# Performance work log

Measured on AMD Instinct MI355X. Metric: run time of the kernel, lower is better.

Reference implementation:

```python
import jax, jax.numpy as jnp
import numpy as np

D, DEPTH, HEADS, P, IMG = 768, 12, 12, 16, 224
GRID = IMG // P
NTOK = GRID * GRID + 1  # 197
PLEN, NTASK, NCLS = 5, 5, 100
DEEP = (2, 3, 4)
HD = D // HEADS
LN_EPS = 1e-6


def _ln(x, w, b):
    m = x.mean(-1, keepdims=True)
    v = ((x - m) ** 2).mean(-1, keepdims=True)
    return (x - m) * jax.lax.rsqrt(v + LN_EPS) * w + b


def _l2n(x):
    return x * jax.lax.rsqrt(jnp.maximum((x * x).sum(-1, keepdims=True), 1e-12))


def _mlp(x, w1, b1, w2, b2):
    return jax.nn.gelu(x @ w1.T + b1, approximate=False) @ w2.T + b2


def _mha(x, wqkv, bqkv, wp, bp):
    B, N, _ = x.shape
    qkv = (x @ wqkv.T + bqkv).reshape(B, N, 3, HEADS, HD)
    q, k, v = qkv[:, :, 0], qkv[:, :, 1], qkv[:, :, 2]
    a = jax.nn.softmax(jnp.einsum('bnhd,bmhd->bhnm', q * HD ** -0.5, k), -1)
    o = jnp.einsum('bhnm,bmhd->bnhd', a, v).reshape(B, N, D)
    return o @ wp.T + bp


def _block(x, i, p):
    x = x + _mha(_ln(x, p['ln1_w'][i], p['ln1_b'][i]), p['qkv_w'][i], p['qkv_b'][i], p['proj_w'][i], p['proj_b'][i])
    return x + _mlp(_ln(x, p['ln2_w'][i], p['ln2_b'][i]), p['fc1_w'][i], p['fc1_b'][i], p['fc2_w'][i], p['fc2_b'][i])


def _blocks(x, p):
    for i in range(DEPTH):
        x = _block(x, i, p)
    return x


def _deep_block(x, i, li, prompts, p):
    # single-head prefix-prompt attention exactly as written in the torch module,
    # including the (buggy but faithful) transpose(1,2).reshape(B,N,C) scramble
    B, N, _ = x.shape
    nx = _ln(x, p['ln1_w'][i], p['ln1_b'][i])
    qkv = (nx @ p['qkv_w'][i].T + p['qkv_b'][i]).reshape(B, N, 3, D)
    q, k, v = qkv[:, :, 0], qkv[:, :, 1], qkv[:, :, 2]
    k = jnp.concatenate([prompts[:, 2 * li], k], axis=1)
    v = jnp.concatenate([prompts[:, 2 * li + 1], v], axis=1)
    a = jax.nn.softmax(jnp.einsum('bnd,bmd->bnm', q, k) * HD ** -0.5, -1)
    av = jnp.einsum('bnm,bmd->bnd', a, v)
    av = av.swapaxes(1, 2).reshape(B, N, D)
    x = x + (av @ p['proj_w'][i].T + p['proj_b'][i])
    return x + _mlp(_ln(x, p['ln2_w'][i], p['ln2_b'][i]), p['fc1_w'][i], p['fc1_b'][i], p['fc2_w'][i], p['fc2_b'][i])


def _embed(inputs, patch_w, patch_b, cls_token, pos_embed):
    B = inputs.shape[0]
    x = inputs.reshape(B, 3, GRID, P, GRID, P).transpose(0, 2, 4, 1, 3, 5).reshape(B, GRID * GRID, 3 * P * P)
    x = x @ patch_w.T + patch_b
    x = jnp.concatenate([jnp.broadcast_to(cls_token, (B, 1, D)), x], axis=1)
    return x + pos_embed


def _branch_forward(x, sel_main, main_idx, sub_idx, p, main_prompts, sub_prompt, pos_embed, fc_w, fc_b, norm_w, norm_b):
    B = x.shape[0]
    # ---- main branch: per-sample gathered deep prompts ----
    mx = x[main_idx]
    mp = main_prompts[sel_main].reshape(mx.shape[0], 2 * len(DEEP), PLEN, D)
    for i in range(DEPTH):
        if i in DEEP:
            mx = _deep_block(mx, i, DEEP.index(i), mp, p)
        else:
            mx = _block(mx, i, p)
    mx = _ln(mx, norm_w, norm_b)
    mlog = mx[:, 0] @ fc_w.T + fc_b  # fc_norm is Identity in timm vit_base
    # ---- sub branch: prepend sub prompts after cls ----
    sx = x[sub_idx]
    sp = jnp.broadcast_to(sub_prompt[0] + pos_embed[0, 0], (sx.shape[0], PLEN, D))
    sx = jnp.concatenate([sx[:, :1], sp, sx[:, 1:]], axis=1)
    sx = _ln(_blocks(sx, p), norm_w, norm_b)
    slog = sx[:, 1:1 + PLEN].mean(axis=1) @ fc_w.T + fc_b
    # scatter back to per-sample logits (fixed output shape)
    return jnp.zeros((B, NCLS), x.dtype).at[main_idx].set(mlog).at[sub_idx].set(slog)


def setup_inputs() -> dict:
    key = jax.random.key(0)
    ks = iter(jax.random.split(key, 32))
    nk = lambda: next(ks)
    r = lambda shape, sc=0.02: jax.random.normal(nk(), shape, jnp.float32) * sc
    return {
        'inputs': jax.random.normal(nk(), (16, 3, IMG, IMG), jnp.float32),
        'task_id': 4,
        'patch_w': r((D, 3 * P * P)),
        'patch_b': jnp.zeros((D,)),
        'cls_token': r((1, 1, D)),
        'pos_embed': r((1, NTOK, D)),
        'qkv_w': r((DEPTH, 3 * D, D)),
        'qkv_b': jnp.zeros((DEPTH, 3 * D)),
        'proj_w': r((DEPTH, D, D)),
        'proj_b': jnp.zeros((DEPTH, D)),
        'ln1_w': jnp.ones((DEPTH, D)), 'ln1_b': jnp.zeros((DEPTH, D)),
        'ln2_w': jnp.ones((DEPTH, D)), 'ln2_b': jnp.zeros((DEPTH, D)),
        'fc1_w': r((DEPTH, 4 * D, D)),
        'fc1_b': jnp.zeros((DEPTH, 4 * D)),
        'fc2_w': r((DEPTH, D, 4 * D)),
        'fc2_b': jnp.zeros((DEPTH, D)),
        'norm_w': jnp.ones((D,)), 'norm_b': jnp.zeros((D,)),
        'fc_w': r((NCLS, D)),
        'fc_b': jnp.zeros((NCLS,)),
        'main_key': r((NTASK, D), 1.0),
        'sub_key': r((1, D), 1.0),
        'main_prompts': r((NTASK, 1, 2, len(DEEP), PLEN, D), 1.0),
        'sub_prompt': r((1, PLEN, D), 1.0),
    }


def reference(inputs, task_id, patch_w, patch_b, cls_token, pos_embed, qkv_w, qkv_b, proj_w, proj_b,
              ln1_w, ln1_b, ln2_w, ln2_b, fc1_w, fc1_b, fc2_w, fc2_b, norm_w, norm_b, fc_w, fc_b,
              main_key, sub_key, main_prompts, sub_prompt):
    p = dict(qkv_w=qkv_w, qkv_b=qkv_b, proj_w=proj_w, proj_b=proj_b, ln1_w=ln1_w, ln1_b=ln1_b,
             ln2_w=ln2_w, ln2_b=ln2_b, fc1_w=fc1_w, fc1_b=fc1_b, fc2_w=fc2_w, fc2_b=fc2_b)
    x = _embed(inputs, patch_w, patch_b, cls_token, pos_embed)
    # frozen query pass (torch.no_grad in the original)
    query = _ln(_blocks(x, p), norm_w, norm_b)[:, 0]
    # test-time routing: cosine similarity to [main_key[:task_id+1], sub_key]
    cand = jnp.concatenate([main_key[:task_id + 1], sub_key], axis=0)
    sim = _l2n(query) @ _l2n(cand).T
    sel = jnp.argmax(sim, axis=1)  # selection_size == 1
    main_mask = sel <= task_id
    main_idx = jnp.nonzero(main_mask)[0]
    sub_idx = jnp.nonzero(jnp.logical_not(main_mask))[0]
    sel_main = sel[main_idx]
    return _branch_forward(x, sel_main, main_idx, sub_idx, p, main_prompts, sub_prompt, pos_embed,
                           fc_w, fc_b, norm_w, norm_b)
```

## Files before the change

### kernel.cpp

```cpp
#include <hip/hip_runtime.h>
#include <math.h>

#define B_    16
#define NT_   197
#define NS_   202
#define HEADS_ 12
#define DEPTH_ 12
#define NCLS_ 100
#define MROW_ (B_ * NT_)
#define SROW_ (B_ * NS_)
#define CROW_ (MROW_ + SROW_)
#define PAD_  128

typedef __attribute__((ext_vector_type(8))) short short8v;
typedef __attribute__((ext_vector_type(4))) float f32x4;

__device__ __forceinline__ short f2bf(float f){
    unsigned u = __builtin_bit_cast(unsigned, f);
    unsigned r = (u + 0x7FFFu + ((u >> 16) & 1u)) >> 16;
    return (short)r;
}
__device__ __forceinline__ unsigned pk2(float a, float b){
    return (unsigned)(unsigned short)f2bf(a) | (((unsigned)(unsigned short)f2bf(b)) << 16);
}
__device__ __forceinline__ float bf2f(unsigned short s){
    unsigned u = ((unsigned)s) << 16;
    return __builtin_bit_cast(float, u);
}
__device__ __forceinline__ float4 ld4bf(const short* p){
    uint2 u = *(const uint2*)p;
    float4 r;
    r.x = bf2f((unsigned short)(u.x & 0xffff));
    r.y = bf2f((unsigned short)(u.x >> 16));
    r.z = bf2f((unsigned short)(u.y & 0xffff));
    r.w = bf2f((unsigned short)(u.y >> 16));
    return r;
}
__device__ __forceinline__ void gld16(const short* g, short* l){
    __builtin_amdgcn_global_load_lds(
        (const __attribute__((address_space(1))) unsigned*)g,
        (__attribute__((address_space(3))) unsigned*)l, 16, 0, 0);
}

__device__ __forceinline__ double block_reduce_sum_d(double s, double* red, int lane, int wid){
#pragma unroll
    for (int off = 32; off; off >>= 1) s += __shfl_xor(s, off);
    if (lane == 0) red[wid] = s;
    __syncthreads();
    double S = red[0] + red[1] + red[2] + red[3];
    __syncthreads();
    return S;
}

__global__ void convert_w_k(const float* __restrict__ in, short* __restrict__ out, long n){
    long i = ((long)blockIdx.x * 256 + threadIdx.x) * 8;
    long stride = (long)gridDim.x * 256 * 8;
    for (; i < n; i += stride){
        float4 a = *(const float4*)(in + i);
        float4 b = *(const float4*)(in + i + 4);
        uint4 o4;
        o4.x = pk2(a.x, a.y); o4.y = pk2(a.z, a.w);
        o4.z = pk2(b.x, b.y); o4.w = pk2(b.z, b.w);
        *(uint4*)(out + i) = o4;
    }
}

template<int EPI, int WB>
__global__ __launch_bounds__(256) void gemm_bf16(
    const short* __restrict__ A, const void* __restrict__ Wv,
    const float* __restrict__ bias, const float* __restrict__ Res,
    float* __restrict__ Cf, short* __restrict__ Cb, int M, int K, int N)
{
    __shared__ short As0[128 * 32];
    __shared__ short As1[128 * 32];
    __shared__ short Bs0[128 * 32];
    __shared__ short Bs1[128 * 32];
    const int t = threadIdx.x;
    const int lane = t & 63, wid = t >> 6;
    const int wr = wid >> 1, wc = wid & 1;
    const long row0 = (long)blockIdx.y * 128;
    const long col0 = (long)blockIdx.x * 128;

    f32x4 acc[4][4];
#pragma unroll
    for (int i = 0; i < 4; i++)
#pragma unroll
        for (int j = 0; j < 4; j++) acc[i][j] = (f32x4){0.f, 0.f, 0.f, 0.f};

    const int l15 = lane & 15, lkg = lane >> 4;
    const int lrow = lane >> 2;
    const int lcol = (lane & 3) * 8;

    for (int k0 = 0; k0 < K; k0 += 64){
#pragma unroll
        for (int i = 0; i < 2; i++){
            int rb = wid * 32 + i * 16;
            const short* gs = A + (row0 + rb + lrow) * K + k0 + lcol;
            gld16(gs,      &As0[rb * 32]);
            gld16(gs + 32, &As1[rb * 32]);
        }
        if (WB == 1){
            const short* Wb = (const short*)Wv;
#pragma unroll
            for (int i = 0; i < 2; i++){
                int rb = wid * 32 + i * 16;
                const short* gs = Wb + (col0 + rb + lrow) * K + k0 + lcol;
                gld16(gs,      &Bs0[rb * 32]);
                gld16(gs + 32, &Bs1[rb * 32]);
            }
        } else {
            const float* Wf = (const float*)Wv;
            const int bn = t >> 1, bh = t & 1;
#pragma unroll
            for (int half = 0; half < 2; half++){
                const float* Wp = Wf + (col0 + bn) * K + k0 + half * 32 + bh * 16;
                unsigned rr[8];
#pragma unroll
                for (int g = 0; g < 8; g++){
                    float2 f = *(const float2*)(Wp + g * 2);
                    rr[g] = pk2(f.x, f.y);
                }
                uint4 lo = {rr[0], rr[1], rr[2], rr[3]};
                uint4 hi = {rr[4], rr[5], rr[6], rr[7]};
                short* Bsh = half ? Bs1 : Bs0;
                *(uint4*)(&Bsh[bn * 32 + bh * 16])     = lo;
                *(uint4*)(&Bsh[bn * 32 + bh * 16 + 8]) = hi;
            }
        }
        __syncthreads();

        {
            short8v a[4], b[4];
#pragma unroll
            for (int i = 0; i < 4; i++)
                a[i] = *(const short8v*)(&As0[(wr * 64 + i * 16 + l15) * 32 + lkg * 8]);
#pragma unroll
            for (int j = 0; j < 4; j++)
                b[j] = *(const short8v*)(&Bs0[(wc * 64 + j * 16 + l15) * 32 + lkg * 8]);
#pragma unroll
            for (int i = 0; i < 4; i++)
#pragma unroll
                for (int j = 0; j < 4; j++)
                    acc[i][j] = __builtin_amdgcn_mfma_f32_16x16x32_bf16(a[i], b[j], acc[i][j], 0, 0, 0);
        }
        {
            short8v a[4], b[4];
#pragma unroll
            for (int i = 0; i < 4; i++)
                a[i] = *(const short8v*)(&As1[(wr * 64 + i * 16 + l15) * 32 + lkg * 8]);
#pragma unroll
            for (int j = 0; j < 4; j++)
                b[j] = *(const short8v*)(&Bs1[(wc * 64 + j * 16 + l15) * 32 + lkg * 8]);
#pragma unroll
            for (int i = 0; i < 4; i++)
#pragma unroll
                for (int j = 0; j < 4; j++)
                    acc[i][j] = __builtin_amdgcn_mfma_f32_16x16x32_bf16(a[i], b[j], acc[i][j], 0, 0, 0);
        }
        __syncthreads();
    }

#pragma unroll
    for (int i = 0; i < 4; i++){
#pragma unroll
        for (int q = 0; q < 4; q++){
            long gr = row0 + wr * 64 + i * 16 + lkg * 4 + q;
            if (gr >= M) continue;
#pragma unroll
            for (int j = 0; j < 4; j++){
                long gc = col0 + wc * 64 + j * 16 + l15;
                float v = acc[i][j][q] + bias[gc];
                if (EPI == 1){
                    v = 0.5f * v * (1.f + erff(v * 0.70710678118654752f));
                    Cb[gr * N + gc] = f2bf(v);
                } else if (EPI == 2){
                    Cf[gr * N + gc] = v + Res[gr * N + gc];
                } else if (EPI == 3){
                    Cb[gr * N + gc] = f2bf(v);
                } else {
                    Cf[gr * N + gc] = v;
                }
            }
        }
    }
}

__global__ __launch_bounds__(256) void ln_k(const float* __restrict__ x,
    const float* __restrict__ w, const float* __restrict__ b,
    short* __restrict__ y, int M)
{
    const int lane = threadIdx.x & 63, wv = threadIdx.x >> 6;
    const int row = blockIdx.x * 4 + wv;
    if (row >= M) return;
    const float* xr = x + (long)row * 768;
    float v[12];
    float s = 0.f;
#pragma unroll
    for (int j = 0; j < 12; j++){ v[j] = xr[lane + j * 64]; s += v[j]; }
#pragma unroll
    for (int off = 32; off; off >>= 1) s += __shfl_xor(s, off);
    float m = s * (1.f / 768.f);
    float q = 0.f;
#pragma unroll
    for (int j = 0; j < 12; j++){ v[j] -= m; q += v[j] * v[j]; }
#pragma unroll
    for (int off = 32; off; off >>= 1) q += __shfl_xor(q, off);
    float rs = 1.f / sqrtf(q * (1.f / 768.f) + 1e-6f);
    short* yr = y + (long)row * 768;
#pragma unroll
    for (int j = 0; j < 12; j++)
        yr[lane + j * 64] = f2bf(v[j] * rs * w[lane + j * 64] + b[lane + j * 64]);
}

__global__ __launch_bounds__(512) void attn_mfma(
    const short* __restrict__ qkv0, short* __restrict__ o0, int N0, int tb0, int te0,
    const short* __restrict__ qkv1, short* __restrict__ o1, int N1, int tb1, int te1)
{
    __shared__ short Ks[208 * 72];
    __shared__ short Vs[64 * 232];
    __shared__ short Ps[8 * 16 * 232];
    const int bh = blockIdx.x;
    const int b = bh / HEADS_, h = bh % HEADS_;
    const int seg = blockIdx.y;
    const short* qkv = seg ? qkv1 : qkv0;
    short* o = seg ? o1 : o0;
    const int Ntok = seg ? N1 : N0;
    const int tb = seg ? tb1 : tb0;
    const int te = seg ? te1 : te0;
    const int t = threadIdx.x, lane = t & 63, wid = t >> 6;
    const long rb = (long)b * Ntok;

    {
        const int r = t >> 2, c = (t & 3) * 16;
#pragma unroll
        for (int pass = 0; pass < 2; pass++){
            int m = r + pass * 128;
            if (m < 208){
                if (m < Ntok){
                    const short* kr = qkv + (rb + m) * 2304 + 768  + h * 64 + c;
                    const short* vr = qkv + (rb + m) * 2304 + 1536 + h * 64 + c;
                    *(uint4*)(&Ks[m * 72 + c])     = *(const uint4*)(kr);
                    *(uint4*)(&Ks[m * 72 + c + 8]) = *(const uint4*)(kr + 8);
#pragma unroll
                    for (int j = 0; j < 16; j++)
                        Vs[(c + j) * 232 + m] = vr[j];
                } else {
#pragma unroll
                    for (int j = 0; j < 16; j += 2)
                        *(unsigned*)(&Ks[m * 72 + c + j]) = 0u;
#pragma unroll
                    for (int j = 0; j < 16; j++)
                        Vs[(c + j) * 232 + m] = 0;
                }
            }
        }
        for (int i = t; i < 64 * 16; i += 512){
            int d = i >> 4, m = 208 + (i & 15);
            Vs[d * 232 + m] = 0;
        }
        for (int i = t; i < 8 * 16 * 16; i += 512){
            int w = i >> 8, rr = (i >> 4) & 15, m = 208 + (i & 15);
            Ps[(w * 16 + rr) * 232 + m] = 0;
        }
    }
    __syncthreads();

    const int l15 = lane & 15, lkg = lane >> 4;
    short* Pw = &Ps[wid * 16 * 232];

    for (int s = tb + wid; s < te; s += 8){
        const int q0 = s * 16;
        short8v a0, a1;
        {
            int qrow = q0 + l15;
            if (qrow < Ntok){
                const short* qp = qkv + (rb + qrow) * 2304 + h * 64;
                a0 = *(const short8v*)(qp + lkg * 8);
                a1 = *(const short8v*)(qp + 32 + lkg * 8);
            } else {
                uint4 z = {0u,0u,0u,0u};
                a0 = __builtin_bit_cast(short8v, z);
                a1 = __builtin_bit_cast(short8v, z);
            }
        }
        f32x4 sacc[13];
#pragma unroll
        for (int j = 0; j < 13; j++){
            short8v b0 = *(const short8v*)(&Ks[(j * 16 + l15) * 72 + lkg * 8]);
            short8v b1 = *(const short8v*)(&Ks[(j * 16 + l15) * 72 + 32 + lkg * 8]);
            f32x4 z = {0.f, 0.f, 0.f, 0.f};
            z = __builtin_amdgcn_mfma_f32_16x16x32_bf16(a0, b0, z, 0, 0, 0);
            z = __builtin_amdgcn_mfma_f32_16x16x32_bf16(a1, b1, z, 0, 0, 0);
            sacc[j][0] = z[0] * 0.125f; sacc[j][1] = z[1] * 0.125f;
            sacc[j][2] = z[2] * 0.125f; sacc[j][3] = z[3] * 0.125f;
        }
#pragma unroll
        for (int j = 0; j < 13; j++){
            if (j * 16 + l15 >= Ntok){
                sacc[j][0] = -1e30f; sacc[j][1] = -1e30f;
                sacc[j][2] = -1e30f; sacc[j][3] = -1e30f;
            }
        }
#pragma unroll
        for (int rr = 0; rr < 4; rr++){
            float mx = sacc[0][rr];
#pragma unroll
            for (int j = 1; j < 13; j++) mx = fmaxf(mx, sacc[j][rr]);
            mx = fmaxf(mx, __shfl_xor(mx, 1));
            mx = fmaxf(mx, __shfl_xor(mx, 2));
            mx = fmaxf(mx, __shfl_xor(mx, 4));
            mx = fmaxf(mx, __shfl_xor(mx, 8));
            float pv[13];
            float sum = 0.f;
#pragma unroll
            for (int j = 0; j < 13; j++){
                float e = expf(sacc[j][rr] - mx);
                pv[j] = e; sum += e;
            }
            sum += __shfl_xor(sum, 1);
            sum += __shfl_xor(sum, 2);
            sum += __shfl_xor(sum, 4);
            sum += __shfl_xor(sum, 8);
            float inv = 1.f / sum;
#pragma unroll
            for (int j = 0; j < 13; j++)
                Pw[(lkg * 4 + rr) * 232 + j * 16 + l15] = f2bf(pv[j] * inv);
        }
        short8v pa[7];
#pragma unroll
        for (int kc = 0; kc < 7; kc++)
            pa[kc] = *(const short8v*)(&Pw[l15 * 232 + kc * 32 + lkg * 8]);
#pragma unroll
        for (int dj = 0; dj < 4; dj++){
            f32x4 oacc = {0.f, 0.f, 0.f, 0.f};
#pragma unroll
            for (int kc = 0; kc < 7; kc++){
                short8v vb = *(const short8v*)(&Vs[(dj * 16 + l15) * 232 + kc * 32 + lkg * 8]);
                oacc = __builtin_amdgcn_mfma_f32_16x16x32_bf16(pa[kc], vb, oacc, 0, 0, 0);
            }
#pragma unroll
            for (int rr = 0; rr < 4; rr++){
                int q = q0 + lkg * 4 + rr;
                if (q < Ntok)
                    o[(rb + q) * 768 + h * 64 + dj * 16 + l15] = f2bf(oacc[rr]);
            }
        }
    }
}

__global__ __launch_bounds__(256) void attn_deep_v3(
    const short* __restrict__ qkv, const float* __restrict__ prompts,
    const int* __restrict__ selm, short* __restrict__ o, int li)
{
    __shared__ float sc[4][208];
    const int b = blockIdx.x, g = blockIdx.y, t = threadIdx.x;
    const int lane = t & 63, w = t >> 6;
    const int n0 = g * 4;

    float4 q0[4], q1[4], q2[4];
#pragma unroll
    for (int qi = 0; qi < 4; qi++){
        int n = n0 + qi;
        int nn = (n < NT_) ? n : (NT_ - 1);
        const short* qr = qkv + (long)(b * NT_ + nn) * 2304;
        q0[qi] = ld4bf(qr + lane * 4);
        q1[qi] = ld4bf(qr + 256 + lane * 4);
        q2[qi] = ld4bf(qr + 512 + lane * 4);
    }

    const float* kp = prompts + ((long)selm[b] * 6 + 2 * li) * 5 * 768;
    const float* vp = kp + 5 * 768;

    for (int m = w; m < 202; m += 4){
        float4 k0, k1, k2;
        if (m < 5){
            const float* kr = kp + (long)m * 768;
            k0 = *(const float4*)(kr + lane * 4);
            k1 = *(const float4*)(kr + 256 + lane * 4);
            k2 = *(const float4*)(kr + 512 + lane * 4);
        } else {
            const short* kr = qkv + (long)(b * NT_ + (m - 5)) * 2304 + 768;
            k0 = ld4bf(kr + lane * 4);
            k1 = ld4bf(kr + 256 + lane * 4);
            k2 = ld4bf(kr + 512 + lane * 4);
        }
        float a[4];
#pragma unroll
        for (int qi = 0; qi < 4; qi++){
            a[qi] = q0[qi].x*k0.x + q0[qi].y*k0.y + q0[qi].z*k0.z + q0[qi].w*k0.w
                  + q1[qi].x*k1.x + q1[qi].y*k1.y + q1[qi].z*k1.z + q1[qi].w*k1.w
                  + q2[qi].x*k2.x + q2[qi].y*k2.y + q2[qi].z*k2.z + q2[qi].w*k2.w;
        }
#pragma unroll
        for (int off = 32; off; off >>= 1){
#pragma unroll
            for (int qi = 0; qi < 4; qi++) a[qi] += __shfl_xor(a[qi], off);
        }
        if (lane == 0){
#pragma unroll
            for (int qi = 0; qi < 4; qi++) sc[qi][m] = a[qi] * 0.125f;
        }
    }
    __syncthreads();

    {
        float v[4];
#pragma unroll
        for (int i = 0; i < 4; i++){
            int m = lane + i * 64;
            v[i] = (m < 202) ? sc[w][m] : -1e30f;
        }
        float mx = fmaxf(fmaxf(v[0], v[1]), fmaxf(v[2], v[3]));
#pragma unroll
        for (int off = 32; off; off >>= 1) mx = fmaxf(mx, __shfl_xor(mx, off));
        float e[4], sum = 0.f;
#pragma unroll
        for (int i = 0; i < 4; i++){
            int m = lane + i * 64;
            e[i] = (m < 202) ? expf(v[i] - mx) : 0.f;
            sum += e[i];
        }
#pragma unroll
        for (int off = 32; off; off >>= 1) sum += __shfl_xor(sum, off);
        float inv = 1.f / sum;
#pragma unroll
        for (int i = 0; i < 4; i++){
            int m = lane + i * 64;
            if (m < 202) sc[w][m] = e[i] * inv;
        }
    }
    __syncthreads();

    float a0[4] = {0.f,0.f,0.f,0.f}, a1[4] = {0.f,0.f,0.f,0.f}, a2[4] = {0.f,0.f,0.f,0.f};
    for (int m = 0; m < 5; m++){
        const float* vr = vp + (long)m * 768;
        float v0 = vr[t], v1 = vr[t + 256], v2 = vr[t + 512];
#pragma unroll
        for (int qi = 0; qi < 4; qi++){
            float pm = sc[qi][m];
            a0[qi] += pm * v0; a1[qi] += pm * v1; a2[qi] += pm * v2;
        }
    }
    for (int m = 5; m < 202; m++){
        const short* vr = qkv + (long)(b * NT_ + (m - 5)) * 2304 + 1536;
        float v0 = bf2f((unsigned short)vr[t]);
        float v1 = bf2f((unsigned short)vr[t + 256]);
        float v2 = bf2f((unsigned short)vr[t + 512]);
#pragma unroll
        for (int qi = 0; qi < 4; qi++){
            float pm = sc[qi][m];
            a0[qi] += pm * v0; a1[qi] += pm * v1; a2[qi] += pm * v2;
        }
    }
#pragma unroll
    for (int qi = 0; qi < 4; qi++){
        int n = n0 + qi;
        if (n < NT_){
            short* ob = o + (long)b * NT_ * 768 + n;
            ob[(long)t * 197]         = f2bf(a0[qi]);
            ob[(long)(t + 256) * 197] = f2bf(a1[qi]);
            ob[(long)(t + 512) * 197] = f2bf(a2[qi]);
        }
    }
}

__global__ void unfold_k(const float* __restrict__ in, short* __restrict__ out){
    long i = (long)blockIdx.x * 256 + threadIdx.x;
    long total = (long)B_ * 196 * 768;
    if (i >= total) return;
    int f = (int)(i % 768); long rw = i / 768;
    int t = (int)(rw % 196); int b = (int)(rw / 196);
    int gy = t / 14, gx = t % 14;
    int c = f >> 8, rem = f & 255, py = rem >> 4, px = rem & 15;
    out[i] = f2bf(in[(((long)(b * 3 + c) * 224) + gy * 16 + py) * 224 + gx * 16 + px]);
}

__global__ void assemble_k(const float* __restrict__ pe, const float* __restrict__ cls,
    const float* __restrict__ pos, float* __restrict__ x0){
    long i = (long)blockIdx.x * 256 + threadIdx.x;
    long total = (long)B_ * NT_ * 768;
    if (i >= total) return;
    int d = (int)(i % 768); long rw = i / 768;
    int n = (int)(rw % NT_); int b = (int)(rw / NT_);
    float v;
    if (n == 0) v = cls[d] + pos[d];
    else        v = pe[((long)b * 196 + (n - 1)) * 768 + d] + pos[(long)n * 768 + d];
    x0[i] = v;
}

__global__ void copy_f(const float* __restrict__ a, float* __restrict__ b, long total){
    long i = (long)blockIdx.x * 256 + threadIdx.x;
    if (i < total) b[i] = a[i];
}

__global__ void build_sub_k(const float* __restrict__ x0, const float* __restrict__ subp,
    const float* __restrict__ pos, float* __restrict__ xSub){
    long i = (long)blockIdx.x * 256 + threadIdx.x;
    long total = (long)B_ * NS_ * 768;
    if (i >= total) return;
    int d = (int)(i % 768); long rw = i / 768;
    int n = (int)(rw % NS_); int b = (int)(rw / NS_);
    float v;
    if (n == 0)      v = x0[((long)b * NT_) * 768 + d];
    else if (n <= 5) v = subp[(n - 1) * 768 + d] + pos[d];
    else             v = x0[((long)b * NT_ + (n - 5)) * 768 + d];
    xSub[i] = v;
}

__global__ __launch_bounds__(256) void select_k(
    const float* __restrict__ xA, const float* __restrict__ norm_w,
    const float* __restrict__ norm_b, const float* __restrict__ main_key,
    const float* __restrict__ sub_key, const int* __restrict__ task_id_p,
    int* __restrict__ selm, int* __restrict__ flag)
{
    __shared__ double red[4];
    int b = blockIdx.x, t = threadIdx.x, lane = t & 63, wid = t >> 6;
    const float* xr = xA + (long)b * NT_ * 768;
    double v0 = xr[t], v1 = xr[t + 256], v2 = xr[t + 512];
    double S = block_reduce_sum_d(v0 + v1 + v2, red, lane, wid);
    double m = S * (1.0 / 768.0);
    double d0 = v0 - m, d1 = v1 - m, d2 = v2 - m;
    double Q = block_reduce_sum_d(d0*d0 + d1*d1 + d2*d2, red, lane, wid);
    double rs = 1.0 / sqrt(Q * (1.0 / 768.0) + 1e-6);
    double q0 = d0 * rs * (double)norm_w[t]       + (double)norm_b[t];
    double q1 = d1 * rs * (double)norm_w[t + 256] + (double)norm_b[t + 256];
    double q2 = d2 * rs * (double)norm_w[t + 512] + (double)norm_b[t + 512];
    double qn = block_reduce_sum_d(q0*q0 + q1*q1 + q2*q2, red, lane, wid);
    double qinv = 1.0 / sqrt(fmax(qn, 1e-12));

    int tk = *task_id_p;
    int ncand = tk + 2;
    double best = -1e300; int bsel = 0;
    for (int c = 0; c < ncand; c++){
        const float* cr = (c <= tk) ? (main_key + (long)c * 768) : sub_key;
        double c0 = cr[t], c1 = cr[t + 256], c2 = cr[t + 512];
        double dotq = block_reduce_sum_d(q0*c0 + q1*c1 + q2*c2, red, lane, wid);
        double nc   = block_reduce_sum_d(c0*c0 + c1*c1 + c2*c2, red, lane, wid);
        double sim = dotq * qinv * (1.0 / sqrt(fmax(nc, 1e-12)));
        if (sim > best){ best = sim; bsel = c; }
    }
    if (t == 0){
        int isMain = (bsel <= tk) ? 1 : 0;
        selm[b] = isMain ? bsel : 0;
        flag[b] = isMain;
    }
}

__global__ __launch_bounds__(256) void head_k(
    const float* __restrict__ xM, const float* __restrict__ xSub,
    const float* __restrict__ norm_w, const float* __restrict__ norm_b,
    const float* __restrict__ fc_w, const float* __restrict__ fc_b,
    const int* __restrict__ flag, float* __restrict__ out)
{
    __shared__ double vec[768];
    __shared__ double red[4];
    int b = blockIdx.x, t = threadIdx.x, lane = t & 63, wid = t >> 6;
    int isMain = flag[b];
    double a0 = 0.0, a1 = 0.0, a2 = 0.0;
    int nrows = isMain ? 1 : 5;
    for (int rI = 0; rI < nrows; rI++){
        const float* xr = isMain ? (xM + (long)b * NT_ * 768)
                                 : (xSub + ((long)b * NS_ + 1 + rI) * 768);
        double v0 = xr[t], v1 = xr[t + 256], v2 = xr[t + 512];
        double S = block_reduce_sum_d(v0 + v1 + v2, red, lane, wid);
        double m = S * (1.0 / 768.0);
        double d0 = v0 - m, d1 = v1 - m, d2 = v2 - m;
        double Q = block_reduce_sum_d(d0*d0 + d1*d1 + d2*d2, red, lane, wid);
        double rs = 1.0 / sqrt(Q * (1.0 / 768.0) + 1e-6);
        a0 += d0 * rs * (double)norm_w[t]       + (double)norm_b[t];
        a1 += d1 * rs * (double)norm_w[t + 256] + (double)norm_b[t + 256];
        a2 += d2 * rs * (double)norm_w[t + 512] + (double)norm_b[t + 512];
    }
    double scl = isMain ? 1.0 : 0.2;
    vec[t] = a0 * scl; vec[t + 256] = a1 * scl; vec[t + 512] = a2 * scl;
    __syncthreads();
    if (t < NCLS_){
        const float* wr = fc_w + (long)t * 768;
        double acc = (double)fc_b[t];
#pragma unroll 8
        for (int j = 0; j < 768; j++) acc += vec[j] * (double)wr[j];
        out[b * NCLS_ + t] = (float)acc;
    }
}

struct Params {
    const float *qkv_w, *qkv_b, *proj_w, *proj_b;
    const float *ln1_w, *ln1_b, *ln2_w, *ln2_b;
    const float *fc1_w, *fc1_b, *fc2_w, *fc2_b;
    const float *prompts; const int* selm;
    short *lnb, *attb, *hidb;
    short *qkvb;
    const short *qkv_wc, *proj_wc, *fc1_wc, *fc2_wc;
    bool cache;
};

template<int EPI>
static void launch_gemm(hipStream_t st, const short* A, const float* Wf, const short* Wc,
                        bool cache, const float* bias, const float* Res,
                        float* Cf, short* Cb, int M, int K, int N)
{
    dim3 g(N / 128, (M + 127) / 128);
    if (cache)
        gemm_bf16<EPI, 1><<<g, 256, 0, st>>>(A, (const void*)Wc, bias, Res, Cf, Cb, M, K, N);
    else
        gemm_bf16<EPI, 0><<<g, 256, 0, st>>>(A, (const void*)Wf, bias, Res, Cf, Cb, M, K, N);
}

static void run_layer(hipStream_t st, float* x, int M, int layer, int mode, int li,
                      const Params& P)
{
    int lnGrid = (M + 3) / 4;
    ln_k<<<lnGrid, 256, 0, st>>>(x, P.ln1_w + layer * 768, P.ln1_b + layer * 768, P.lnb, M);
    launch_gemm<3>(st, P.lnb, P.qkv_w + (long)layer * 2304 * 768,
        P.qkv_wc + (P.cache ? (long)layer * 2304 * 768 : 0), P.cache,
        P.qkv_b + layer * 2304, nullptr, nullptr, P.qkvb, M, 768, 2304);
    if (mode == 0){
        attn_mfma<<<dim3(B_ * HEADS_, 2), 512, 0, st>>>(
            P.qkvb, P.attb, NT_, 0, 13,
            P.qkvb + (long)MROW_ * 2304, P.attb + (long)MROW_ * 768, NS_, 0, 13);
    } else if (mode == 1){
        attn_mfma<<<dim3(B_ * HEADS_, 2), 512, 0, st>>>(
            P.qkvb, P.attb, NT_, 0, 7,
            P.qkvb, P.attb, NT_, 7, 13);
    } else {
        attn_deep_v3<<<dim3(B_, 50), 256, 0, st>>>(P.qkvb, P.prompts, P.selm, P.attb, li);
    }
    launch_gemm<2>(st, P.attb, P.proj_w + (long)layer * 768 * 768,
        P.proj_wc + (P.cache ? (long)layer * 768 * 768 : 0), P.cache,
        P.proj_b + layer * 768, x, x, nullptr, M, 768, 768);
    ln_k<<<lnGrid, 256, 0, st>>>(x, P.ln2_w + layer * 768, P.ln2_b + layer * 768, P.lnb, M);
    launch_gemm<1>(st, P.lnb, P.fc1_w + (long)layer * 3072 * 768,
        P.fc1_wc + (P.cache ? (long)layer * 3072 * 768 : 0), P.cache,
        P.fc1_b + layer * 3072, nullptr, nullptr, P.hidb, M, 768, 3072);
    launch_gemm<2>(st, P.hidb, P.fc2_w + (long)layer * 768 * 3072,
        P.fc2_wc + (P.cache ? (long)layer * 768 * 3072 : 0), P.cache,
        P.fc2_b + layer * 768, x, x, nullptr, M, 3072, 768);
}

extern "C" void kernel_launch(void* const* d_in, const int* in_sizes, int n_in,
                              void* d_out, int out_size, void* d_ws, size_t ws_size,
                              hipStream_t stream)
{
    (void)in_sizes; (void)n_in; (void)out_size;
    const float* inputs   = (const float*)d_in[0];
    const int*   task_id  = (const int*)  d_in[1];
    const float* patch_w  = (const float*)d_in[2];
    const float* patch_b  = (const float*)d_in[3];
    const float* cls_tok  = (const float*)d_in[4];
    const float* pos      = (const float*)d_in[5];
    const float* qkv_w    = (const float*)d_in[6];
    const float* qkv_b    = (const float*)d_in[7];
    const float* proj_w   = (const float*)d_in[8];
    const float* proj_b   = (const float*)d_in[9];
    const float* ln1_w    = (const float*)d_in[10];
    const float* ln1_b    = (const float*)d_in[11];
    const float* ln2_w    = (const float*)d_in[12];
    const float* ln2_b    = (const float*)d_in[13];
    const float* fc1_w    = (const float*)d_in[14];
    const float* fc1_b    = (const float*)d_in[15];
    const float* fc2_w    = (const float*)d_in[16];
    const float* fc2_b    = (const float*)d_in[17];
    const float* norm_w   = (const float*)d_in[18];
    const float* norm_b   = (const float*)d_in[19];
    const float* fc_w     = (const float*)d_in[20];
    const float* fc_b     = (const float*)d_in[21];
    const float* main_key = (const float*)d_in[22];
    const float* sub_key  = (const float*)d_in[23];
    const float* m_prompts= (const float*)d_in[24];
    const float* s_prompt = (const float*)d_in[25];
    float* out = (float*)d_out;

    char* wsb = (char*)d_ws;
    size_t off = 0;
    auto allocB = [&](size_t bytes) -> void* {
        void* p = (void*)(wsb + off);
        off += (bytes + 255) & ~(size_t)255;
        return p;
    };
    float* x0   = (float*)allocB((size_t)MROW_ * 768 * 4);
    float* xC   = (float*)allocB((size_t)CROW_ * 768 * 4);
    float* xM   = (float*)allocB((size_t)MROW_ * 768 * 4);
    short* lnb  = (short*)allocB((size_t)(CROW_ + PAD_) * 768 * 2);
    short* attb = (short*)allocB((size_t)(CROW_ + PAD_) * 768 * 2);
    short* qkvb = (short*)allocB((size_t)(CROW_ + PAD_) * 2304 * 2);
    short* hidb = (short*)allocB((size_t)(CROW_ + PAD_) * 3072 * 2);
    float* peo  = (float*)allocB((size_t)3136 * 768 * 4);
    int*   selm = (int*)allocB(64);
    int*   flag = (int*)allocB(64);

    const size_t nQkv = (size_t)DEPTH_ * 2304 * 768;
    const size_t nProj = (size_t)DEPTH_ * 768 * 768;
    const size_t nFc1 = (size_t)DEPTH_ * 3072 * 768;
    const size_t nFc2 = (size_t)DEPTH_ * 768 * 3072;
    const size_t nPatch = (size_t)768 * 768;
    size_t cacheBytes = (nQkv + nProj + nFc1 + nFc2 + nPatch) * 2 + 5 * 256;
    bool cache = (ws_size >= off + cacheBytes + (1u << 20));
    short *qkv_wc = nullptr, *proj_wc = nullptr, *fc1_wc = nullptr, *fc2_wc = nullptr, *patch_wc = nullptr;
    if (cache){
        qkv_wc  = (short*)allocB(nQkv * 2);
        proj_wc = (short*)allocB(nProj * 2);
        fc1_wc  = (short*)allocB(nFc1 * 2);
        fc2_wc  = (short*)allocB(nFc2 * 2);
        patch_wc= (short*)allocB(nPatch * 2);
        convert_w_k<<<2048, 256, 0, stream>>>(qkv_w,  qkv_wc,  (long)nQkv);
        convert_w_k<<<1024, 256, 0, stream>>>(proj_w, proj_wc, (long)nProj);
        convert_w_k<<<2048, 256, 0, stream>>>(fc1_w,  fc1_wc,  (long)nFc1);
        convert_w_k<<<2048, 256, 0, stream>>>(fc2_w,  fc2_wc,  (long)nFc2);
        convert_w_k<<<256,  256, 0, stream>>>(patch_w, patch_wc, (long)nPatch);
    }

    Params P;
    P.qkv_w = qkv_w; P.qkv_b = qkv_b; P.proj_w = proj_w; P.proj_b = proj_b;
    P.ln1_w = ln1_w; P.ln1_b = ln1_b; P.ln2_w = ln2_w; P.ln2_b = ln2_b;
    P.fc1_w = fc1_w; P.fc1_b = fc1_b; P.fc2_w = fc2_w; P.fc2_b = fc2_b;
    P.prompts = m_prompts; P.selm = selm;
    P.lnb = lnb; P.attb = attb; P.hidb = hidb; P.qkvb = qkvb;
    P.qkv_wc = qkv_wc; P.proj_wc = proj_wc; P.fc1_wc = fc1_wc; P.fc2_wc = fc2_wc;
    P.cache = cache;

    const long XN = (long)MROW_ * 768;

    {
        long tot = (long)B_ * 196 * 768;
        short* un = hidb;
        unfold_k<<<(int)((tot + 255) / 256), 256, 0, stream>>>(inputs, un);
        launch_gemm<0>(stream, un, patch_w, patch_wc, cache, patch_b, nullptr,
                       peo, nullptr, 3136, 768, 768);
        assemble_k<<<(int)((XN + 255) / 256), 256, 0, stream>>>(peo, cls_tok, pos, x0);
        copy_f<<<(int)((XN + 255) / 256), 256, 0, stream>>>(x0, xC, XN);
        long st = (long)SROW_ * 768;
        build_sub_k<<<(int)((st + 255) / 256), 256, 0, stream>>>(x0, s_prompt, pos,
                                                                 xC + (long)MROW_ * 768);
    }

    for (int i = 0; i < DEPTH_; i++){
        run_layer(stream, xC, CROW_, i, 0, 0, P);
        if (i == 1)
            copy_f<<<(int)((XN + 255) / 256), 256, 0, stream>>>(xC, xM, XN);
    }

    select_k<<<16, 256, 0, stream>>>(xC, norm_w, norm_b, main_key, sub_key,
                                     task_id, selm, flag);

    for (int i = 2; i < DEPTH_; i++){
        int mode = (i >= 2 && i <= 4) ? 2 : 1;
        run_layer(stream, xM, MROW_, i, mode, i - 2, P);
    }

    head_k<<<16, 256, 0, stream>>>(xM, xC + (long)MROW_ * 768, norm_w, norm_b,
                                   fc_w, fc_b, flag, out);
}
```

Measured before the change: 5.435 ms.

## Compute only consumed token rows after attention in final layers

```diff
diff --git a/kernel.cpp b/kernel.cpp
--- a/kernel.cpp
+++ b/kernel.cpp
@@ -11,6 +11,8 @@
 #define SROW_ (B_ * NS_)
 #define CROW_ (MROW_ + SROW_)
 #define PAD_  128
+#define TAILC_ 96
+#define TAILM_ 16
 
 typedef __attribute__((ext_vector_type(8))) short short8v;
 typedef __attribute__((ext_vector_type(4))) float f32x4;
@@ -464,6 +466,29 @@
     }
 }
 
+__device__ __forceinline__ long tail_src_row(int r, int mode){
+    if (mode == 1) return (long)r * NT_;
+    if (r < 16)    return (long)r * NT_;
+    int j = r - 16;
+    return (long)MROW_ + (long)(j / 5) * NS_ + 1 + (j % 5);
+}
+__global__ void gather_tail_f(const float* __restrict__ src, float* __restrict__ dst,
+                              int nrows, int mode){
+    long i = (long)blockIdx.x * 256 + threadIdx.x;
+    long total = (long)nrows * 768;
+    if (i >= total) return;
+    int r = (int)(i / 768), d = (int)(i % 768);
+    dst[i] = src[tail_src_row(r, mode) * 768 + d];
+}
+__global__ void gather_tail_b(const short* __restrict__ src, short* __restrict__ dst,
+                              int nrows, int mode){
+    long i = (long)blockIdx.x * 256 + threadIdx.x;
+    long total = (long)nrows * 768;
+    if (i >= total) return;
+    int r = (int)(i / 768), d = (int)(i % 768);
+    dst[i] = src[tail_src_row(r, mode) * 768 + d];
+}
+
 __global__ void unfold_k(const float* __restrict__ in, short* __restrict__ out){
     long i = (long)blockIdx.x * 256 + threadIdx.x;
     long total = (long)B_ * 196 * 768;
@@ -508,14 +533,14 @@
 }
 
 __global__ __launch_bounds__(256) void select_k(
-    const float* __restrict__ xA, const float* __restrict__ norm_w,
+    const float* __restrict__ xT, const float* __restrict__ norm_w,
     const float* __restrict__ norm_b, const float* __restrict__ main_key,
     const float* __restrict__ sub_key, const int* __restrict__ task_id_p,
     int* __restrict__ selm, int* __restrict__ flag)
 {
     __shared__ double red[4];
     int b = blockIdx.x, t = threadIdx.x, lane = t & 63, wid = t >> 6;
-    const float* xr = xA + (long)b * NT_ * 768;
+    const float* xr = xT + (long)b * 768;
     double v0 = xr[t], v1 = xr[t + 256], v2 = xr[t + 512];
     double S = block_reduce_sum_d(v0 + v1 + v2, red, lane, wid);
     double m = S * (1.0 / 768.0);
@@ -547,7 +572,7 @@
 }
 
 __global__ __launch_bounds__(256) void head_k(
-    const float* __restrict__ xM, const float* __restrict__ xSub,
+    const float* __restrict__ xMT, const float* __restrict__ xT,
     const float* __restrict__ norm_w, const float* __restrict__ norm_b,
     const float* __restrict__ fc_w, const float* __restrict__ fc_b,
     const int* __restrict__ flag, float* __restrict__ out)
@@ -559,8 +584,8 @@
     double a0 = 0.0, a1 = 0.0, a2 = 0.0;
     int nrows = isMain ? 1 : 5;
     for (int rI = 0; rI < nrows; rI++){
-        const float* xr = isMain ? (xM + (long)b * NT_ * 768)
-                                 : (xSub + ((long)b * NS_ + 1 + rI) * 768);
+        const float* xr = isMain ? (xMT + (long)b * 768)
+                                 : (xT + (long)(16 + b * 5 + rI) * 768);
         double v0 = xr[t], v1 = xr[t + 256], v2 = xr[t + 512];
         double S = block_reduce_sum_d(v0 + v1 + v2, red, lane, wid);
         double m = S * (1.0 / 768.0);
@@ -592,6 +617,8 @@
     short *qkvb;
     const short *qkv_wc, *proj_wc, *fc1_wc, *fc2_wc;
     bool cache;
+    float *xT, *xMT;
+    short *attbT, *lnbT, *hidT;
 };
 
 template<int EPI>
@@ -635,6 +662,41 @@
     launch_gemm<2>(st, P.hidb, P.fc2_w + (long)layer * 768 * 3072,
         P.fc2_wc + (P.cache ? (long)layer * 768 * 3072 : 0), P.cache,
         P.fc2_b + layer * 768, x, x, nullptr, M, 3072, 768);
+}
+
+static void run_layer_tail(hipStream_t st, float* x, int M, int layer, int gmode,
+                           const Params& P)
+{
+    int lnGrid = (M + 3) / 4;
+    ln_k<<<lnGrid, 256, 0, st>>>(x, P.ln1_w + layer * 768, P.ln1_b + layer * 768, P.lnb, M);
+    launch_gemm<3>(st, P.lnb, P.qkv_w + (long)layer * 2304 * 768,
+        P.qkv_wc + (P.cache ? (long)layer * 2304 * 768 : 0), P.cache,
+        P.qkv_b + layer * 2304, nullptr, nullptr, P.qkvb, M, 768, 2304);
+    if (gmode == 0){
+        attn_mfma<<<dim3(B_ * HEADS_, 2), 512, 0, st>>>(
+            P.qkvb, P.attb, NT_, 0, 1,
+            P.qkvb + (long)MROW_ * 2304, P.attb + (long)MROW_ * 768, NS_, 0, 1);
+    } else {
+        attn_mfma<<<dim3(B_ * HEADS_, 1), 512, 0, st>>>(
+            P.qkvb, P.attb, NT_, 0, 1,
+            P.qkvb, P.attb, NT_, 0, 1);
+    }
+    const int Mt = (gmode == 0) ? TAILC_ : TAILM_;
+    float* xt = (gmode == 0) ? P.xT : P.xMT;
+    long tot = (long)Mt * 768;
+    gather_tail_f<<<(int)((tot + 255) / 256), 256, 0, st>>>(x, xt, Mt, gmode);
+    gather_tail_b<<<(int)((tot + 255) / 256), 256, 0, st>>>(P.attb, P.attbT, Mt, gmode);
+    launch_gemm<2>(st, P.attbT, P.proj_w + (long)layer * 768 * 768,
+        P.proj_wc + (P.cache ? (long)layer * 768 * 768 : 0), P.cache,
+        P.proj_b + layer * 768, xt, xt, nullptr, Mt, 768, 768);
+    ln_k<<<(Mt + 3) / 4, 256, 0, st>>>(xt, P.ln2_w + layer * 768, P.ln2_b + layer * 768,
+                                       P.lnbT, Mt);
+    launch_gemm<1>(st, P.lnbT, P.fc1_w + (long)layer * 3072 * 768,
+        P.fc1_wc + (P.cache ? (long)layer * 3072 * 768 : 0), P.cache,
+        P.fc1_b + layer * 3072, nullptr, nullptr, P.hidT, Mt, 768, 3072);
+    launch_gemm<2>(st, P.hidT, P.fc2_w + (long)layer * 768 * 3072,
+        P.fc2_wc + (P.cache ? (long)layer * 768 * 3072 : 0), P.cache,
+        P.fc2_b + layer * 768, xt, xt, nullptr, Mt, 3072, 768);
 }
 
 extern "C" void kernel_launch(void* const* d_in, const int* in_sizes, int n_in,
@@ -685,6 +747,11 @@
     short* qkvb = (short*)allocB((size_t)(CROW_ + PAD_) * 2304 * 2);
     short* hidb = (short*)allocB((size_t)(CROW_ + PAD_) * 3072 * 2);
     float* peo  = (float*)allocB((size_t)3136 * 768 * 4);
+    float* xT    = (float*)allocB((size_t)TAILC_ * 768 * 4);
+    float* xMT   = (float*)allocB((size_t)TAILM_ * 768 * 4);
+    short* attbT = (short*)allocB((size_t)(TAILC_ + PAD_) * 768 * 2);
+    short* lnbT  = (short*)allocB((size_t)(TAILC_ + PAD_) * 768 * 2);
+    short* hidT  = (short*)allocB((size_t)(TAILC_ + PAD_) * 3072 * 2);
     int*   selm = (int*)allocB(64);
     int*   flag = (int*)allocB(64);
 
@@ -717,6 +784,7 @@
     P.lnb = lnb; P.attb = attb; P.hidb = hidb; P.qkvb = qkvb;
     P.qkv_wc = qkv_wc; P.proj_wc = proj_wc; P.fc1_wc = fc1_wc; P.fc2_wc = fc2_wc;
     P.cache = cache;
+    P.xT = xT; P.xMT = xMT; P.attbT = attbT; P.lnbT = lnbT; P.hidT = hidT;
 
     const long XN = (long)MROW_ * 768;
 
@@ -733,20 +801,21 @@
                                                                  xC + (long)MROW_ * 768);
     }
 
-    for (int i = 0; i < DEPTH_; i++){
+    for (int i = 0; i < DEPTH_ - 1; i++){
         run_layer(stream, xC, CROW_, i, 0, 0, P);
         if (i == 1)
             copy_f<<<(int)((XN + 255) / 256), 256, 0, stream>>>(xC, xM, XN);
     }
-
-    select_k<<<16, 256, 0, stream>>>(xC, norm_w, norm_b, main_key, sub_key,
+    run_layer_tail(stream, xC, CROW_, DEPTH_ - 1, 0, P);
+
+    select_k<<<16, 256, 0, stream>>>(xT, norm_w, norm_b, main_key, sub_key,
                                      task_id, selm, flag);
 
-    for (int i = 2; i < DEPTH_; i++){
+    for (int i = 2; i < DEPTH_ - 1; i++){
         int mode = (i >= 2 && i <= 4) ? 2 : 1;
         run_layer(stream, xM, MROW_, i, mode, i - 2, P);
     }
-
-    head_k<<<16, 256, 0, stream>>>(xM, xC + (long)MROW_ * 768, norm_w, norm_b,
-                                   fc_w, fc_b, flag, out);
-}
+    run_layer_tail(stream, xM, MROW_, DEPTH_ - 1, 1, P);
+
+    head_k<<<16, 256, 0, stream>>>(xMT, xT, norm_w, norm_b, fc_w, fc_b, flag, out);
+}
```

After: 5.343 ms. No clear change (-1.7%).
